# Kernel tuning notes

Measured on AMD Instinct MI355X. Metric: run time of the kernel, lower is better.

The kernel has to match this reference:

```python
import jax, jax.numpy as jnp
import numpy as np

HEADS = 8
DIM_HEAD = 64
DIM = 512
HIDDEN = HEADS * DIM_HEAD  # 512


def setup_inputs() -> dict:
    key = jax.random.key(0)
    k1, k2, k3, k4 = jax.random.split(key, 4)
    b, m, n = 4, 8, 512
    x = jax.random.normal(k1, (b, m, n, DIM), dtype=jnp.float32)
    pos_bias = jax.random.normal(k2, (HEADS, n, 16, 16), dtype=jnp.float32)
    # torch nn.Linear(dim, 3*hidden) weight is [3*hidden, dim]; we store the
    # transposed matmul form [dim, 3*hidden] for y = x @ W.
    w_qkv = jax.random.normal(k3, (DIM, 3 * HIDDEN), dtype=jnp.float32) * (DIM ** -0.5)
    w_out = jax.random.normal(k4, (HIDDEN, DIM), dtype=jnp.float32) * (HIDDEN ** -0.5)
    return {"x": x, "pos_bias": pos_bias, "w_qkv": w_qkv, "w_out": w_out}


def reference(x, pos_bias, w_qkv, w_out):
    b, m, n, _ = x.shape
    h, d = HEADS, DIM_HEAD
    scale = d ** -0.5
    qkv = jnp.einsum('bmnc,ce->bmne', x, w_qkv)  # [b,m,n,3*hidden]
    q, k, v = jnp.split(qkv, 3, axis=-1)
    # 'b m n (h d) -> (b m) h n d'
    def to_heads(t):
        return t.reshape(b * m, n, h, d).transpose(0, 2, 1, 3)
    q, k, v = to_heads(q), to_heads(k), to_heads(v)
    q = q * scale
    sim = jnp.einsum('bhid,bhjd->bhij', q, k)  # [(b*m), h, n, n]
    # pos_bias [h, n, p, q] -> mean over last two dims -> [h, n] -> broadcast [1,h,n,1]
    pb = pos_bias.mean(axis=(-2, -1))[None, :, :, None]
    sim = sim + pb
    sim = sim - jax.lax.stop_gradient(jnp.max(sim, axis=-1, keepdims=True))
    attn = jax.nn.softmax(sim, axis=-1)
    out = jnp.einsum('bhij,bhjd->bhid', attn, v)  # [(b*m), h, n, d]
    # '(b m) h n d -> b m n (h d)'
    out = out.transpose(0, 2, 1, 3).reshape(b, m, n, h * d)
    return jnp.einsum('bmne,ec->bmnc', out, w_out)
```

## Files before the change

### kernel.cpp

```cpp
#include <hip/hip_runtime.h>
#include <stdint.h>


typedef __attribute__((ext_vector_type(8))) short bf16x8;
typedef __attribute__((ext_vector_type(4))) float f32x4;
typedef __attribute__((ext_vector_type(4))) unsigned short us4;
typedef __attribute__((ext_vector_type(4))) float float4v;

__device__ __forceinline__ unsigned short f2b(float f) {
  union { float f; uint32_t u; } x; x.f = f;
  uint32_t r = x.u + 0x7fffu + ((x.u >> 16) & 1u);
  return (unsigned short)(r >> 16);
}

__device__ __forceinline__ uint32_t cvtpk(float lo, float hi) {
  uint32_t r;
  asm("v_cvt_pk_bf16_f32 %0, %1, %2" : "=v"(r) : "v"(lo), "v"(hi));
  return r;
}

__device__ __forceinline__ f32x4 mfma16(bf16x8 a, bf16x8 b, f32x4 c) {
  return __builtin_amdgcn_mfma_f32_16x16x32_bf16(a, b, c, 0, 0, 0);
}

__device__ __forceinline__ void gload_lds16(const unsigned short* g, unsigned short* l) {
  __builtin_amdgcn_global_load_lds(
      (const __attribute__((address_space(1))) unsigned int*)g,
      (__attribute__((address_space(3))) unsigned int*)l, 16, 0, 0);
}

__global__ __launch_bounds__(256) void cast_x_kernel(
    const float* __restrict__ src, unsigned short* __restrict__ dst) {
  size_t i = ((size_t)blockIdx.x * 256 + threadIdx.x) * 4;
  float4v v = *(const float4v*)(src + i);
  us4 o;
#pragma unroll
  for (int j = 0; j < 4; ++j) o[j] = f2b(v[j]);
  *(us4*)(dst + i) = o;
}

__global__ __launch_bounds__(256) void transpose_cast_kernel(
    const float* __restrict__ src, unsigned short* __restrict__ dst, int R, int C) {
  __shared__ float tile[64][65];
  const int tc0 = blockIdx.x * 64;
  const int tr0 = blockIdx.y * 64;
#pragma unroll
  for (int k2 = 0; k2 < 16; ++k2) {
    int idx = threadIdx.x + k2 * 256;
    int r = idx >> 6, c = idx & 63;
    tile[r][c] = src[(size_t)(tr0 + r) * C + tc0 + c];
  }
  __syncthreads();
#pragma unroll
  for (int k2 = 0; k2 < 16; ++k2) {
    int idx = threadIdx.x + k2 * 256;
    int c = idx >> 6, r = idx & 63;
    dst[(size_t)(tc0 + c) * R + tr0 + r] = f2b(tile[r][c]);
  }
}

__device__ __forceinline__ void gemm_core(
    const unsigned short* __restrict__ A, const unsigned short* __restrict__ Bt,
    int r0, int c0, unsigned short* As, unsigned short* Bs,
    f32x4 (&acc)[4][4]) {
  const int tid = threadIdx.x;
  const int lane = tid & 63;
  const int wave = tid >> 6;
  const int wr = (wave >> 1) * 64;
  const int wc = (wave & 1) * 64;
  const int l15 = lane & 15;
  const int g = lane >> 4;
  const int lsw = l15 & 7;

#pragma unroll
  for (int m = 0; m < 4; ++m)
#pragma unroll
    for (int n = 0; n < 4; ++n) acc[m][n] = (f32x4){0.f, 0.f, 0.f, 0.f};

  auto stage = [&](int kt, int b) {
#pragma unroll
    for (int i = 0; i < 4; ++i) {
      int chunk = tid + i * 512;
      int row = chunk >> 3;
      int csw = (chunk & 7) ^ (row & 7);
      gload_lds16(A + (size_t)(r0 + row) * 512 + kt + csw * 8,
                  As + b * 16384 + chunk * 8);
    }
#pragma unroll
    for (int i = 0; i < 2; ++i) {
      int chunk = tid + i * 512;
      int row = chunk >> 3;
      int csw = (chunk & 7) ^ (row & 7);
      gload_lds16(Bt + (size_t)(c0 + row) * 512 + kt + csw * 8,
                  Bs + b * 8192 + chunk * 8);
    }
  };

  stage(0, 0);
  stage(64, 1);

#pragma unroll
  for (int t = 0; t < 8; ++t) {
    if (t < 7) asm volatile("s_waitcnt vmcnt(6)" ::: "memory");
    else       asm volatile("s_waitcnt vmcnt(0)" ::: "memory");
    __builtin_amdgcn_s_barrier();
    if (t < 6) stage((t + 2) * 64, (t + 2) % 3);
    const unsigned short* as = As + (t % 3) * 16384;
    const unsigned short* bs = Bs + (t % 3) * 8192;
#pragma unroll
    for (int ks = 0; ks < 2; ++ks) {
      bf16x8 af[4], bfr[4];
      const int cj = ((g + ks * 4) ^ lsw) * 8;
#pragma unroll
      for (int m = 0; m < 4; ++m)
        af[m] = *(const bf16x8*)(as + (wr + m * 16 + l15) * 64 + cj);
#pragma unroll
      for (int n = 0; n < 4; ++n)
        bfr[n] = *(const bf16x8*)(bs + (wc + n * 16 + l15) * 64 + cj);
      __builtin_amdgcn_s_setprio(1);
#pragma unroll
      for (int m = 0; m < 4; ++m)
#pragma unroll
        for (int n = 0; n < 4; ++n) acc[m][n] = mfma16(af[m], bfr[n], acc[m][n]);
      __builtin_amdgcn_s_setprio(0);
    }
  }
  __syncthreads();
}

__global__ __launch_bounds__(512, 1) void gemm_qkv_kernel(
    const unsigned short* __restrict__ xb, const unsigned short* __restrict__ wqbT,
    unsigned short* __restrict__ qb, unsigned short* __restrict__ kb,
    unsigned short* __restrict__ vtb) {
  __shared__ unsigned short As[49152];
  __shared__ unsigned short Bs[24576];
  f32x4 acc[4][4];
  const int r0 = blockIdx.x * 256;
  const int c0 = blockIdx.y * 128;
  gemm_core(xb, wqbT, r0, c0, As, Bs, acc);

  const int tid = threadIdx.x, lane = tid & 63, wave = tid >> 6;
  const int wr = (wave >> 1) * 64, wc = (wave & 1) * 64;
  const int l15 = lane & 15, g = lane >> 4;
  const int part = c0 >> 9;
  const float scl = (part == 0) ? 0.125f : 1.0f;

  if (part < 2) {
#pragma unroll
    for (int m = 0; m < 4; ++m) {
      int rbase = wr + m * 16 + 4 * g;
#pragma unroll
      for (int n = 0; n < 4; ++n) {
        int c = wc + n * 16 + l15;
        int c2 = c >> 3, ci = c & 7;
#pragma unroll
        for (int rr = 0; rr < 4; ++rr) {
          int r = rbase + rr;
          As[r * 128 + ((c2 ^ (r & 15)) << 3) + ci] = f2b(acc[m][n][rr] * scl);
        }
      }
    }
    __syncthreads();
    unsigned short* dstb = (part == 0) ? qb : kb;
#pragma unroll
    for (int it = 0; it < 8; ++it) {
      int idx = tid + it * 512;
      int r = idx >> 4, c2 = idx & 15;
      bf16x8 v = *(const bf16x8*)(As + r * 128 + ((c2 ^ (r & 15)) << 3));
      int e = c0 + c2 * 8;
      int rem = e & 511, h = rem >> 6, d = rem & 63;
      int ig = r0 + r;
      int bh = (ig >> 9) * 8 + h, i = ig & 511;
      *(bf16x8*)(dstb + ((size_t)bh * 512 + i) * 64 + d) = v;
    }
  } else {
#pragma unroll
    for (int m = 0; m < 4; ++m) {
      int rbase = wr + m * 16 + 4 * g;
      int r2 = rbase >> 3, rhalf = rbase & 7;
#pragma unroll
      for (int n = 0; n < 4; ++n) {
        int c = wc + n * 16 + l15;
        us4 v;
#pragma unroll
        for (int rr = 0; rr < 4; ++rr) v[rr] = f2b(acc[m][n][rr]);
        *(us4*)(As + c * 256 + ((r2 ^ (c & 31)) << 3) + rhalf) = v;
      }
    }
    __syncthreads();
#pragma unroll
    for (int it = 0; it < 8; ++it) {
      int idx = tid + it * 512;
      int c = idx >> 5, r8 = idx & 31;
      bf16x8 v = *(const bf16x8*)(As + c * 256 + ((r8 ^ (c & 31)) << 3));
      int e = c0 + c;
      int rem = e & 511, h = rem >> 6, d = rem & 63;
      int ig0 = r0 + r8 * 8;
      int bh = (ig0 >> 9) * 8 + h, i = ig0 & 511;
      *(bf16x8*)(vtb + ((size_t)bh * 64 + d) * 512 + i) = v;
    }
  }
}

__global__ __launch_bounds__(512, 1) void gemm_out_kernel(
    const unsigned short* __restrict__ ao, const unsigned short* __restrict__ wobT,
    float* __restrict__ out) {
  __shared__ unsigned short As[49152];
  __shared__ unsigned short Bs[24576];
  f32x4 acc[4][4];
  const int r0 = blockIdx.x * 256;
  const int c0 = blockIdx.y * 128;
  gemm_core(ao, wobT, r0, c0, As, Bs, acc);

  const int tid = threadIdx.x, lane = tid & 63, wave = tid >> 6;
  const int wr = (wave >> 1) * 64, wc = (wave & 1) * 64;
  const int l15 = lane & 15, g = lane >> 4;
#pragma unroll
  for (int m = 0; m < 4; ++m) {
    int i0g = r0 + wr + m * 16 + 4 * g;
#pragma unroll
    for (int n = 0; n < 4; ++n) {
      int e = c0 + wc + n * 16 + l15;
#pragma unroll
      for (int rr = 0; rr < 4; ++rr)
        out[(size_t)(i0g + rr) * 512 + e] = acc[m][n][rr];
    }
  }
}

__global__ __launch_bounds__(512, 4) void attn_kernel(
    const unsigned short* __restrict__ qb, const unsigned short* __restrict__ kb,
    const unsigned short* __restrict__ vtb, unsigned short* __restrict__ ao) {
  __shared__ unsigned short kbuf[2][8192];
  __shared__ unsigned short vbuf[2][8192];
  __shared__ unsigned short Ps[8][16][40];
  const int bh = blockIdx.x;
  const int qt = blockIdx.y;
  const int tid = threadIdx.x, lane = tid & 63, wave = tid >> 6;
  const int l15 = lane & 15, g = lane >> 4;
  const int qrow0 = qt * 128 + wave * 16;

  const unsigned short* Q = qb + ((size_t)bh * 512 + qrow0) * 64;
  const unsigned short* Kp = kb + (size_t)bh * 512 * 64;
  const unsigned short* Vt = vtb + (size_t)bh * 64 * 512;

  bf16x8 qf0 = *(const bf16x8*)(Q + l15 * 64 + g * 8);
  bf16x8 qf1 = *(const bf16x8*)(Q + l15 * 64 + 32 + g * 8);

  const int krow = tid >> 3;
  const int kck = (tid & 7) ^ (krow & 7);
  const int vrow = tid >> 4;
  const int vck = (tid & 15) ^ (vrow & 15);

  auto stage = [&](int t, int b) {
    const unsigned short* ks = Kp + ((size_t)t * 128 + krow) * 64 + kck * 8;
    gload_lds16(ks, kbuf[b] + tid * 8);
    gload_lds16(ks + 64 * 64, kbuf[b] + tid * 8 + 4096);
    const unsigned short* vs = Vt + (size_t)vrow * 512 + t * 128 + vck * 8;
    gload_lds16(vs, vbuf[b] + tid * 8);
    gload_lds16(vs + 32 * 512, vbuf[b] + tid * 8 + 4096);
  };

  f32x4 oacc[4];
#pragma unroll
  for (int m = 0; m < 4; ++m) oacc[m] = (f32x4){0.f, 0.f, 0.f, 0.f};
  float srow[4] = {0.f, 0.f, 0.f, 0.f};

  stage(0, 0);
  asm volatile("s_waitcnt vmcnt(0)" ::: "memory");
  __builtin_amdgcn_s_barrier();

  int cur = 0;
#pragma unroll
  for (int t = 0; t < 4; ++t) {
    if (t < 3) stage(t + 1, cur ^ 1);

    const unsigned short* kb_ = kbuf[cur];
    f32x4 s[8];
    const int c0i = g ^ (l15 & 7);
    __builtin_amdgcn_s_setprio(1);
#pragma unroll
    for (int tt = 0; tt < 8; ++tt) {
      int row = tt * 16 + l15;
      bf16x8 b0 = *(const bf16x8*)(kb_ + (row * 8 + c0i) * 8);
      bf16x8 b1 = *(const bf16x8*)(kb_ + (row * 8 + (c0i ^ 4)) * 8);
      f32x4 c = (f32x4){0.f, 0.f, 0.f, 0.f};
      c = mfma16(qf0, b0, c);
      s[tt] = mfma16(qf1, b1, c);
    }
    __builtin_amdgcn_s_setprio(0);

#pragma unroll
    for (int tt = 0; tt < 8; ++tt)
#pragma unroll
      for (int rr = 0; rr < 4; ++rr) {
        float e = __expf(s[tt][rr]);
        s[tt][rr] = e;
        srow[rr] += e;
      }

    const unsigned short* vb_ = vbuf[cur];
#pragma unroll
    for (int cc = 0; cc < 4; ++cc) {
#pragma unroll
      for (int rr = 0; rr < 4; ++rr) {
        uint32_t pk = cvtpk(s[cc * 2][rr], s[cc * 2 + 1][rr]);
        Ps[wave][4 * g + rr][l15] = (unsigned short)pk;
        Ps[wave][4 * g + rr][16 + l15] = (unsigned short)(pk >> 16);
      }
      asm volatile("s_waitcnt lgkmcnt(0)" ::: "memory");
      bf16x8 pf = *(const bf16x8*)(&Ps[wave][l15][g * 8]);
      __builtin_amdgcn_s_setprio(1);
#pragma unroll
      for (int m = 0; m < 4; ++m) {
        int vr = m * 16 + l15;
        bf16x8 vf = *(const bf16x8*)(vb_ + (vr * 16 + ((cc * 4 + g) ^ l15)) * 8);
        oacc[m] = mfma16(vf, pf, oacc[m]);
      }
      __builtin_amdgcn_s_setprio(0);
    }

    if (t < 3) {
      asm volatile("s_waitcnt vmcnt(0)" ::: "memory");
      __builtin_amdgcn_s_barrier();
      cur ^= 1;
    }
  }

#pragma unroll
  for (int rr = 0; rr < 4; ++rr)
#pragma unroll
    for (int o = 1; o < 16; o <<= 1) srow[rr] += __shfl_xor(srow[rr], o);
  int srcl = (l15 >> 2) * 16;
  float t0 = __shfl(srow[0], srcl), t1 = __shfl(srow[1], srcl);
  float t2 = __shfl(srow[2], srcl), t3 = __shfl(srow[3], srcl);
  int rq = l15 & 3;
  float sq = rq == 0 ? t0 : rq == 1 ? t1 : rq == 2 ? t2 : t3;
  float invq = 1.0f / sq;

  const int hh = bh & 7, bm = bh >> 3;
  unsigned short* aorow = ao + ((size_t)bm * 512 + qrow0 + l15) * 512 + hh * 64;
#pragma unroll
  for (int m = 0; m < 4; ++m) {
    union { us4 u; uint32_t w[2]; } uv;
    uv.w[0] = cvtpk(oacc[m][0] * invq, oacc[m][1] * invq);
    uv.w[1] = cvtpk(oacc[m][2] * invq, oacc[m][3] * invq);
    *(us4*)(aorow + m * 16 + 4 * g) = uv.u;
  }
}

extern "C" void kernel_launch(void* const* d_in, const int* in_sizes, int n_in,
                              void* d_out, int out_size, void* d_ws, size_t ws_size,
                              hipStream_t stream) {
  const float* x = (const float*)d_in[0];
  const float* w_qkv = (const float*)d_in[2];
  const float* w_out = (const float*)d_in[3];
  float* out = (float*)d_out;

  char* ws = (char*)d_ws;
  const size_t SZ_XB = 16384ull * 512 * 2;
  const size_t SZ_WQ = 1536ull * 512 * 2;
  const size_t SZ_WO = 512ull * 512 * 2;
  const size_t SZ_HB = 256ull * 512 * 64 * 2;
  unsigned short* xb = (unsigned short*)(ws);
  unsigned short* wqbT = (unsigned short*)(ws + SZ_XB);
  unsigned short* wobT = (unsigned short*)(ws + SZ_XB + SZ_WQ);
  unsigned short* qb = (unsigned short*)(ws + SZ_XB + SZ_WQ + SZ_WO);
  unsigned short* kb = (unsigned short*)(ws + SZ_XB + SZ_WQ + SZ_WO + SZ_HB);
  unsigned short* vtb = (unsigned short*)(ws + SZ_XB + SZ_WQ + SZ_WO + 2 * SZ_HB);
  unsigned short* ao = (unsigned short*)(ws + SZ_XB + SZ_WQ + SZ_WO + 3 * SZ_HB);

  cast_x_kernel<<<8192, 256, 0, stream>>>(x, xb);
  transpose_cast_kernel<<<dim3(1536 / 64, 512 / 64), 256, 0, stream>>>(w_qkv, wqbT, 512, 1536);
  transpose_cast_kernel<<<dim3(512 / 64, 512 / 64), 256, 0, stream>>>(w_out, wobT, 512, 512);
  gemm_qkv_kernel<<<dim3(64, 12), 512, 0, stream>>>(xb, wqbT, qb, kb, vtb);
  attn_kernel<<<dim3(256, 4), 512, 0, stream>>>(qb, kb, vtb, ao);
  gemm_out_kernel<<<dim3(64, 4), 512, 0, stream>>>(ao, wobT, out);
}
```

Baseline: 99.41 us.

## Merge prep kernels and software-pipeline GEMM LDS fragment reads with split staging

Merges the x cast and both weight transpose-casts into one launch, cutting two kernel launches. The shared GEMM core is restructured so the LDS fragment reads for the next k-step overlap the MFMAs of the current one, with register double-buffering. Global-to-LDS staging is split into halves interleaved with compute, with finer waitcnt and barrier points. This adds register pressure and extra barriers, and the hand-tuned vmcnt accounting must match the number of loads in flight.

```diff
diff --git a/kernel.cpp b/kernel.cpp
--- a/kernel.cpp
+++ b/kernel.cpp
@@ -29,21 +29,32 @@
       (__attribute__((address_space(3))) unsigned int*)l, 16, 0, 0);
 }
 
-__global__ __launch_bounds__(256) void cast_x_kernel(
-    const float* __restrict__ src, unsigned short* __restrict__ dst) {
-  size_t i = ((size_t)blockIdx.x * 256 + threadIdx.x) * 4;
-  float4v v = *(const float4v*)(src + i);
-  us4 o;
-#pragma unroll
-  for (int j = 0; j < 4; ++j) o[j] = f2b(v[j]);
-  *(us4*)(dst + i) = o;
-}
-
-__global__ __launch_bounds__(256) void transpose_cast_kernel(
-    const float* __restrict__ src, unsigned short* __restrict__ dst, int R, int C) {
+__global__ __launch_bounds__(256) void prep_kernel(
+    const float* __restrict__ x, unsigned short* __restrict__ xb,
+    const float* __restrict__ wq, unsigned short* __restrict__ wqbT,
+    const float* __restrict__ wo, unsigned short* __restrict__ wobT) {
+  const int bid = blockIdx.x;
+  if (bid < 8192) {
+    size_t i = ((size_t)bid * 256 + threadIdx.x) * 4;
+    float4v v = *(const float4v*)(x + i);
+    us4 o;
+#pragma unroll
+    for (int j = 0; j < 4; ++j) o[j] = f2b(v[j]);
+    *(us4*)(xb + i) = o;
+    return;
+  }
   __shared__ float tile[64][65];
-  const int tc0 = blockIdx.x * 64;
-  const int tr0 = blockIdx.y * 64;
+  const float* src;
+  unsigned short* dst;
+  int R, C, bx, by;
+  if (bid < 8192 + 192) {
+    int q = bid - 8192;
+    src = wq; dst = wqbT; R = 512; C = 1536; bx = q % 24; by = q / 24;
+  } else {
+    int q = bid - 8384;
+    src = wo; dst = wobT; R = 512; C = 512; bx = q % 8; by = q / 8;
+  }
+  const int tc0 = bx * 64, tr0 = by * 64;
 #pragma unroll
   for (int k2 = 0; k2 < 16; ++k2) {
     int idx = threadIdx.x + k2 * 256;
@@ -77,18 +88,17 @@
 #pragma unroll
     for (int n = 0; n < 4; ++n) acc[m][n] = (f32x4){0.f, 0.f, 0.f, 0.f};
 
-  auto stage = [&](int kt, int b) {
-#pragma unroll
-    for (int i = 0; i < 4; ++i) {
-      int chunk = tid + i * 512;
+  auto stage_half = [&](int kt, int b, int h) {
+#pragma unroll
+    for (int i = 0; i < 2; ++i) {
+      int chunk = tid + (h * 2 + i) * 512;
       int row = chunk >> 3;
       int csw = (chunk & 7) ^ (row & 7);
       gload_lds16(A + (size_t)(r0 + row) * 512 + kt + csw * 8,
                   As + b * 16384 + chunk * 8);
     }
-#pragma unroll
-    for (int i = 0; i < 2; ++i) {
-      int chunk = tid + i * 512;
+    {
+      int chunk = tid + h * 512;
       int row = chunk >> 3;
       int csw = (chunk & 7) ^ (row & 7);
       gload_lds16(Bt + (size_t)(c0 + row) * 512 + kt + csw * 8,
@@ -96,34 +106,53 @@
     }
   };
 
-  stage(0, 0);
-  stage(64, 1);
+  auto readfr = [&](const unsigned short* as, const unsigned short* bs, int ks,
+                    bf16x8 (&af)[4], bf16x8 (&bf)[4]) {
+    const int cj = ((g + ks * 4) ^ lsw) * 8;
+#pragma unroll
+    for (int m = 0; m < 4; ++m)
+      af[m] = *(const bf16x8*)(as + (wr + m * 16 + l15) * 64 + cj);
+#pragma unroll
+    for (int n = 0; n < 4; ++n)
+      bf[n] = *(const bf16x8*)(bs + (wc + n * 16 + l15) * 64 + cj);
+  };
+
+  auto domfma = [&](bf16x8 (&af)[4], bf16x8 (&bf)[4]) {
+    __builtin_amdgcn_s_setprio(1);
+#pragma unroll
+    for (int m = 0; m < 4; ++m)
+#pragma unroll
+      for (int n = 0; n < 4; ++n) acc[m][n] = mfma16(af[m], bf[n], acc[m][n]);
+    __builtin_amdgcn_s_setprio(0);
+  };
+
+  stage_half(0, 0, 0);  stage_half(0, 0, 1);
+  stage_half(64, 1, 0); stage_half(64, 1, 1);
+  asm volatile("s_waitcnt vmcnt(6)" ::: "memory");
+  __builtin_amdgcn_s_barrier();
+
+  bf16x8 fa[2][4], fb[2][4];
+  readfr(As, Bs, 0, fa[0], fb[0]);
 
 #pragma unroll
   for (int t = 0; t < 8; ++t) {
-    if (t < 7) asm volatile("s_waitcnt vmcnt(6)" ::: "memory");
-    else       asm volatile("s_waitcnt vmcnt(0)" ::: "memory");
-    __builtin_amdgcn_s_barrier();
-    if (t < 6) stage((t + 2) * 64, (t + 2) % 3);
     const unsigned short* as = As + (t % 3) * 16384;
     const unsigned short* bs = Bs + (t % 3) * 8192;
-#pragma unroll
-    for (int ks = 0; ks < 2; ++ks) {
-      bf16x8 af[4], bfr[4];
-      const int cj = ((g + ks * 4) ^ lsw) * 8;
-#pragma unroll
-      for (int m = 0; m < 4; ++m)
-        af[m] = *(const bf16x8*)(as + (wr + m * 16 + l15) * 64 + cj);
-#pragma unroll
-      for (int n = 0; n < 4; ++n)
-        bfr[n] = *(const bf16x8*)(bs + (wc + n * 16 + l15) * 64 + cj);
-      __builtin_amdgcn_s_setprio(1);
-#pragma unroll
-      for (int m = 0; m < 4; ++m)
-#pragma unroll
-        for (int n = 0; n < 4; ++n) acc[m][n] = mfma16(af[m], bfr[n], acc[m][n]);
-      __builtin_amdgcn_s_setprio(0);
-    }
+    readfr(as, bs, 1, fa[1], fb[1]);
+    if (t + 2 < 8) stage_half((t + 2) * 64, (t + 2) % 3, 0);
+    __builtin_amdgcn_s_barrier();
+    domfma(fa[0], fb[0]);
+    if (t + 1 < 8) {
+      if (t + 2 < 8) asm volatile("s_waitcnt vmcnt(3)" ::: "memory");
+      else           asm volatile("s_waitcnt vmcnt(0)" ::: "memory");
+      __builtin_amdgcn_s_barrier();
+      const unsigned short* as2 = As + ((t + 1) % 3) * 16384;
+      const unsigned short* bs2 = Bs + ((t + 1) % 3) * 8192;
+      readfr(as2, bs2, 0, fa[0], fb[0]);
+      if (t + 2 < 8) stage_half((t + 2) * 64, (t + 2) % 3, 1);
+    }
+    domfma(fa[1], fb[1]);
+    __builtin_amdgcn_s_barrier();
   }
   __syncthreads();
 }
@@ -370,9 +399,7 @@
   unsigned short* vtb = (unsigned short*)(ws + SZ_XB + SZ_WQ + SZ_WO + 2 * SZ_HB);
   unsigned short* ao = (unsigned short*)(ws + SZ_XB + SZ_WQ + SZ_WO + 3 * SZ_HB);
 
-  cast_x_kernel<<<8192, 256, 0, stream>>>(x, xb);
-  transpose_cast_kernel<<<dim3(1536 / 64, 512 / 64), 256, 0, stream>>>(w_qkv, wqbT, 512, 1536);
-  transpose_cast_kernel<<<dim3(512 / 64, 512 / 64), 256, 0, stream>>>(w_out, wobT, 512, 512);
+  prep_kernel<<<8448, 256, 0, stream>>>(x, xb, w_qkv, wqbT, w_out, wobT);
   gemm_qkv_kernel<<<dim3(64, 12), 512, 0, stream>>>(xb, wqbT, qb, kb, vtb);
   attn_kernel<<<dim3(256, 4), 512, 0, stream>>>(qb, kb, vtb, ao);
   gemm_out_kernel<<<dim3(64, 4), 512, 0, stream>>>(ao, wobT, out);
```

After: 97.95 us. No clear change (-1.5%).
